# Kernel optimization log

Hardware: AMD Instinct MI355X
Metric: run time of the kernel (lower is better)

## Reference

```python
import jax, jax.numpy as jnp
import numpy as np

B, S, E = 8, 2048, 1024
H, DK = 128, 8  # embed_dim = H * DK; DK = n_wires per quantum head


def setup_inputs() -> dict:
    key = jax.random.key(0)
    k1, k2, k3, k4 = jax.random.split(key, 4)
    x = jax.random.normal(k1, (B, S, E), dtype=jnp.float32)
    theta = jax.random.normal(k2, (H, DK), dtype=jnp.float32)  # trainable RX angles per head/wire
    W = jax.random.normal(k3, (E, E), dtype=jnp.float32) * (1.0 / np.sqrt(E))
    b = jax.random.normal(k4, (E,), dtype=jnp.float32) * 0.01
    return {"x": x, "theta": theta, "W": W, "b": b}


def reference(x, theta, W, b):
    # Quantum circuit per token/head: RX(x_i) then RX(theta_i) on wire i starting
    # from |0...0>. Single-qubit RX gates compose: RX(a)RX(b)=RX(a+b), and
    # <Z> after RX(angle)|0> = cos(angle). So the MeasureAll(PauliZ) output is
    # cos(x_i + theta_i) elementwise -- fully vectorized over batch/seq/head/wire.
    Bx, Sx, Ex = x.shape
    Hx, dk = theta.shape
    xs = x.reshape(Bx, Sx, Hx, dk)            # [B,S,H,dk]
    head_out = jnp.cos(xs + theta[None, None])  # [B,S,H,dk]
    out = head_out.reshape(Bx, Sx, Ex)
    return out @ W.T + b                       # combine Linear
```

## Files before the change

kernel.cpp:

```cpp
#include <hip/hip_runtime.h>
#include <hip/hip_bf16.h>
#include <stdint.h>

#define M_DIM 16384
#define N_DIM 1024
#define K_DIM 1024

typedef __attribute__((ext_vector_type(8))) short short8;
typedef __attribute__((ext_vector_type(16))) float f32x16;

#define GLD_LDS(g, l) __builtin_amdgcn_global_load_lds( \
    (const __attribute__((address_space(1))) unsigned int*)(g), \
    (__attribute__((address_space(3))) unsigned int*)(l), 16, 0, 0)

__device__ __forceinline__ unsigned short f2bf(float f) {
  union { float f; unsigned int u; } v;
  v.f = f;
  unsigned int u = v.u + 0x7FFFu + ((v.u >> 16) & 1u);
  return (unsigned short)(u >> 16);
}

#define PREP_A_BLOCKS (M_DIM * K_DIM / 2048)
#define PREP_W_BLOCKS (N_DIM * K_DIM / 2048)
__global__ __launch_bounds__(256) void prep_all(const float* __restrict__ x,
                                                const float* __restrict__ theta,
                                                const float* __restrict__ W,
                                                unsigned short* __restrict__ A,
                                                unsigned short* __restrict__ Wb) {
  const int tid = threadIdx.x;
  if (blockIdx.x < PREP_A_BLOCKS) {
    const long base = (long)blockIdx.x * 2048;
    const float4 t = *(const float4*)(theta + tid * 4);
#pragma unroll
    for (int p = 0; p < 2; ++p) {
      const long i = base + p * 1024 + tid * 4;
      const float4 xv = *(const float4*)(x + i);
      ushort4 o;
      o.x = f2bf(__cosf(xv.x + t.x));
      o.y = f2bf(__cosf(xv.y + t.y));
      o.z = f2bf(__cosf(xv.z + t.z));
      o.w = f2bf(__cosf(xv.w + t.w));
      *(ushort4*)(A + i) = o;
    }
  } else {
    const long base = (long)(blockIdx.x - PREP_A_BLOCKS) * 2048;
#pragma unroll
    for (int p = 0; p < 2; ++p) {
      const long i = base + p * 1024 + tid * 4;
      const float4 wv = *(const float4*)(W + i);
      ushort4 o;
      o.x = f2bf(wv.x);
      o.y = f2bf(wv.y);
      o.z = f2bf(wv.z);
      o.w = f2bf(wv.w);
      *(ushort4*)(Wb + i) = o;
    }
  }
}

__global__ __launch_bounds__(256) void gemm_bt(const unsigned short* __restrict__ A,
                                               const unsigned short* __restrict__ Bt,
                                               const float* __restrict__ bias,
                                               float* __restrict__ C) {
  constexpr int BM = 128, BN = 128, BK = 64;
  __shared__ unsigned short As[BM * BK];
  __shared__ unsigned short Bs[BN * BK];
  const int tid = threadIdx.x;

  const int L = blockIdx.y * 8 + blockIdx.x;
  const int bx = (L >> 3) & 7;
  const int by = (L & 7) * 16 + (L >> 6);
  const int m0 = by * BM;
  const int n0 = bx * BN;

  const int lane = tid & 63;
  const int wave = tid >> 6;
  const int wm = (wave >> 1) * 64;
  const int wn = (wave & 1) * 64;

  f32x16 acc[2][2] = {};

  const int srow = tid >> 3;
  const int scol = ((tid & 7) ^ (srow & 7)) * 8;
  const unsigned short* Ag = A + (long)(m0 + srow) * K_DIM + scol;
  const unsigned short* Bg = Bt + (long)(n0 + srow) * K_DIM + scol;
  unsigned short* Asd = As + tid * 8;
  unsigned short* Bsd = Bs + tid * 8;

  const int fr = lane & 31;
  const int kh = (lane >> 5) * 8;

  for (int k0 = 0; k0 < K_DIM; k0 += BK) {
    __syncthreads();
#pragma unroll
    for (int i = 0; i < 4; ++i)
      GLD_LDS(Ag + (long)i * 32 * K_DIM, Asd + i * 2048);
#pragma unroll
    for (int i = 0; i < 4; ++i)
      GLD_LDS(Bg + (long)i * 32 * K_DIM, Bsd + i * 2048);
    Ag += BK;
    Bg += BK;
    __syncthreads();

#pragma unroll
    for (int ks = 0; ks < 4; ++ks) {
      const int c = (ks * 16 + kh) >> 3;
      short8 af[2], bf[2];
#pragma unroll
      for (int i = 0; i < 2; ++i) {
        const int r = wm + i * 32 + fr;
        af[i] = *(const short8*)(As + r * BK + (c ^ (r & 7)) * 8);
      }
#pragma unroll
      for (int j = 0; j < 2; ++j) {
        const int r = wn + j * 32 + fr;
        bf[j] = *(const short8*)(Bs + r * BK + (c ^ (r & 7)) * 8);
      }
#pragma unroll
      for (int i = 0; i < 2; ++i)
#pragma unroll
        for (int j = 0; j < 2; ++j)
          acc[i][j] = __builtin_amdgcn_mfma_f32_32x32x16_bf16(af[i], bf[j], acc[i][j], 0, 0, 0);
    }
  }

  const int cn = lane & 31;
  const int rbase = (lane >> 5) * 4;
#pragma unroll
  for (int j = 0; j < 2; ++j) {
    const int n = n0 + wn + j * 32 + cn;
    const float bv = bias[n];
#pragma unroll
    for (int i = 0; i < 2; ++i) {
      const long mrow = (long)(m0 + wm + i * 32 + rbase);
#pragma unroll
      for (int r = 0; r < 16; ++r) {
        const long row = mrow + (r & 3) + 8 * (r >> 2);
        C[row * N_DIM + n] = acc[i][j][r] + bv;
      }
    }
  }
}

extern "C" void kernel_launch(void* const* d_in, const int* in_sizes, int n_in,
                              void* d_out, int out_size, void* d_ws, size_t ws_size,
                              hipStream_t stream) {
  const float* x = (const float*)d_in[0];
  const float* theta = (const float*)d_in[1];
  const float* W = (const float*)d_in[2];
  const float* b = (const float*)d_in[3];
  float* out = (float*)d_out;

  unsigned short* Abf = (unsigned short*)d_ws;
  unsigned short* Wbf = Abf + (size_t)M_DIM * K_DIM;

  hipLaunchKernelGGL(prep_all, dim3(PREP_A_BLOCKS + PREP_W_BLOCKS), dim3(256), 0,
                     stream, x, theta, W, Abf, Wbf);
  hipLaunchKernelGGL(gemm_bt, dim3(N_DIM / 128, M_DIM / 128), dim3(256), 0, stream,
                     Abf, Wbf, b, out);
}
```

Baseline: 157.5 us.

## Double-buffer LDS tiles and switch GEMM to 16x16x32 MFMA with BK=32

Restructures the GEMM main loop to keep two BK=32 LDS buffers, so global-to-LDS loads for the next K slice are issued before computing on the current one. The 32x32x16 MFMA tiles become 16x16x32 MFMAs over a 4x4 accumulator grid per wave, with a new XOR swizzle matched to the 32-wide K rows. The intent is to hide global load latency behind compute and drop one barrier's worth of idle time per slice. The cost is a smaller K step with more iterations and barriers, plus a different output-store pattern that writes 16-wide column segments.

```diff
diff --git a/kernel.cpp b/kernel.cpp
--- a/kernel.cpp
+++ b/kernel.cpp
@@ -7,7 +7,7 @@
 #define K_DIM 1024
 
 typedef __attribute__((ext_vector_type(8))) short short8;
-typedef __attribute__((ext_vector_type(16))) float f32x16;
+typedef __attribute__((ext_vector_type(4))) float f32x4;
 
 #define GLD_LDS(g, l) __builtin_amdgcn_global_load_lds( \
     (const __attribute__((address_space(1))) unsigned int*)(g), \
@@ -62,84 +62,94 @@
                                                const unsigned short* __restrict__ Bt,
                                                const float* __restrict__ bias,
                                                float* __restrict__ C) {
-  constexpr int BM = 128, BN = 128, BK = 64;
-  __shared__ unsigned short As[BM * BK];
-  __shared__ unsigned short Bs[BN * BK];
+  constexpr int BM = 128, BK = 32;
+  __shared__ unsigned short As[2 * BM * BK];
+  __shared__ unsigned short Bs[2 * BM * BK];
   const int tid = threadIdx.x;
 
   const int L = blockIdx.y * 8 + blockIdx.x;
   const int bx = (L >> 3) & 7;
   const int by = (L & 7) * 16 + (L >> 6);
   const int m0 = by * BM;
-  const int n0 = bx * BN;
+  const int n0 = bx * BM;
 
   const int lane = tid & 63;
   const int wave = tid >> 6;
   const int wm = (wave >> 1) * 64;
   const int wn = (wave & 1) * 64;
 
-  f32x16 acc[2][2] = {};
+  f32x4 acc[4][4] = {};
 
-  const int srow = tid >> 3;
-  const int scol = ((tid & 7) ^ (srow & 7)) * 8;
+  const int srow = tid >> 2;
+  const int scol = ((tid & 3) ^ ((tid >> 3) & 3)) * 8;
   const unsigned short* Ag = A + (long)(m0 + srow) * K_DIM + scol;
   const unsigned short* Bg = Bt + (long)(n0 + srow) * K_DIM + scol;
   unsigned short* Asd = As + tid * 8;
   unsigned short* Bsd = Bs + tid * 8;
 
-  const int fr = lane & 31;
-  const int kh = (lane >> 5) * 8;
+#define STAGE(buf, koff) \
+  do { \
+    GLD_LDS(Ag + (koff), Asd + (buf) * 4096); \
+    GLD_LDS(Ag + (koff) + 64 * K_DIM, Asd + (buf) * 4096 + 2048); \
+    GLD_LDS(Bg + (koff), Bsd + (buf) * 4096); \
+    GLD_LDS(Bg + (koff) + 64 * K_DIM, Bsd + (buf) * 4096 + 2048); \
+  } while (0)
 
-  for (int k0 = 0; k0 < K_DIM; k0 += BK) {
+  const int c = lane >> 4;
+  const int fr = lane & 15;
+
+#define COMPUTE(buf) \
+  do { \
+    const unsigned short* Ab = As + (buf) * 4096; \
+    const unsigned short* Bb = Bs + (buf) * 4096; \
+    short8 af[4], bf[4]; \
+    _Pragma("unroll") \
+    for (int i = 0; i < 4; ++i) { \
+      const int r = wm + i * 16 + fr; \
+      af[i] = *(const short8*)(Ab + r * BK + ((c ^ ((r >> 1) & 3)) * 8)); \
+    } \
+    _Pragma("unroll") \
+    for (int j = 0; j < 4; ++j) { \
+      const int r = wn + j * 16 + fr; \
+      bf[j] = *(const short8*)(Bb + r * BK + ((c ^ ((r >> 1) & 3)) * 8)); \
+    } \
+    _Pragma("unroll") \
+    for (int i = 0; i < 4; ++i) \
+      _Pragma("unroll") \
+      for (int j = 0; j < 4; ++j) \
+        acc[i][j] = __builtin_amdgcn_mfma_f32_16x16x32_bf16(af[i], bf[j], acc[i][j], 0, 0, 0); \
+  } while (0)
+
+  STAGE(0, 0);
+
+#pragma unroll 2
+  for (int it = 0; it < 16; ++it) {
+    const int k2 = it * 2 * BK;
     __syncthreads();
+    STAGE(1, k2 + BK);
+    COMPUTE(0);
+    __syncthreads();
+    if (it < 15)
+      STAGE(0, k2 + 2 * BK);
+    COMPUTE(1);
+  }
+
+  const int cn = lane & 15;
+  const int rq = (lane >> 4) * 4;
 #pragma unroll
-    for (int i = 0; i < 4; ++i)
-      GLD_LDS(Ag + (long)i * 32 * K_DIM, Asd + i * 2048);
+  for (int j = 0; j < 4; ++j) {
+    const int n = n0 + wn + j * 16 + cn;
+    const float bv = bias[n];
 #pragma unroll
-    for (int i = 0; i < 4; ++i)
-      GLD_LDS(Bg + (long)i * 32 * K_DIM, Bsd + i * 2048);
-    Ag += BK;
-    Bg += BK;
-    __syncthreads();
-
+    for (int i = 0; i < 4; ++i) {
+      const long mb = (long)(m0 + wm + i * 16 + rq) * N_DIM + n;
 #pragma unroll
-    for (int ks = 0; ks < 4; ++ks) {
-      const int c = (ks * 16 + kh) >> 3;
-      short8 af[2], bf[2];
-#pragma unroll
-      for (int i = 0; i < 2; ++i) {
-        const int r = wm + i * 32 + fr;
-        af[i] = *(const short8*)(As + r * BK + (c ^ (r & 7)) * 8);
-      }
-#pragma unroll
-      for (int j = 0; j < 2; ++j) {
-        const int r = wn + j * 32 + fr;
-        bf[j] = *(const short8*)(Bs + r * BK + (c ^ (r & 7)) * 8);
-      }
-#pragma unroll
-      for (int i = 0; i < 2; ++i)
-#pragma unroll
-        for (int j = 0; j < 2; ++j)
-          acc[i][j] = __builtin_amdgcn_mfma_f32_32x32x16_bf16(af[i], bf[j], acc[i][j], 0, 0, 0);
+      for (int r = 0; r < 4; ++r)
+        C[mb + (long)r * N_DIM] = acc[i][j][r] + bv;
     }
   }
-
-  const int cn = lane & 31;
-  const int rbase = (lane >> 5) * 4;
-#pragma unroll
-  for (int j = 0; j < 2; ++j) {
-    const int n = n0 + wn + j * 32 + cn;
-    const float bv = bias[n];
-#pragma unroll
-    for (int i = 0; i < 2; ++i) {
-      const long mrow = (long)(m0 + wm + i * 32 + rbase);
-#pragma unroll
-      for (int r = 0; r < 16; ++r) {
-        const long row = mrow + (r & 3) + 8 * (r >> 2);
-        C[row * N_DIM + n] = acc[i][j][r] + bv;
-      }
-    }
-  }
+#undef STAGE
+#undef COMPUTE
 }
 
 extern "C" void kernel_launch(void* const* d_in, const int* in_sizes, int n_in,
```

Measured after the change: 169.4 us. 1.08x slower.
